# Kernel tuning notes

Hardware: AMD Instinct MI355X
Metric: run time of the kernel (lower is better)

## Reference

```python
import jax, jax.numpy as jnp
import numpy as np

N_NODES = 50000
N_EDGES = 800000
D_IN = 128
D_HID = 256
N_CLASSES = 2
N_GRAPHS = 256


def _graph_conv(x, src, dst, W_root, W_rel, b, num_nodes):
    # PyG GraphConv: out_i = W_root @ x_i + W_rel @ sum_{j->i} x_j + b
    agg = jax.ops.segment_sum(x[src], dst, num_segments=num_nodes)  # [N, d_in]
    return x @ W_root.T + agg @ W_rel.T + b


def setup_inputs() -> dict:
    key = jax.random.key(0)
    ks = jax.random.split(key, 12)
    x = jax.random.normal(ks[0], (N_NODES, D_IN), dtype=jnp.float32)
    edge_index = jax.random.randint(ks[1], (2, N_EDGES), 0, N_NODES, dtype=jnp.int64)
    batch = jnp.sort(jax.random.randint(ks[2], (N_NODES,), 0, N_GRAPHS, dtype=jnp.int64))
    s1 = 1.0 / np.sqrt(D_IN)
    s2 = 1.0 / np.sqrt(D_HID)
    W1_root = jax.random.uniform(ks[3], (D_HID, D_IN), minval=-s1, maxval=s1, dtype=jnp.float32)
    W1_rel = jax.random.uniform(ks[4], (D_HID, D_IN), minval=-s1, maxval=s1, dtype=jnp.float32)
    b1 = jax.random.uniform(ks[5], (D_HID,), minval=-s1, maxval=s1, dtype=jnp.float32)
    W2_root = jax.random.uniform(ks[6], (D_HID, D_HID), minval=-s2, maxval=s2, dtype=jnp.float32)
    W2_rel = jax.random.uniform(ks[7], (D_HID, D_HID), minval=-s2, maxval=s2, dtype=jnp.float32)
    b2 = jax.random.uniform(ks[8], (D_HID,), minval=-s2, maxval=s2, dtype=jnp.float32)
    Wfc = jax.random.uniform(ks[9], (N_CLASSES, D_HID), minval=-s2, maxval=s2, dtype=jnp.float32)
    bfc = jax.random.uniform(ks[10], (N_CLASSES,), minval=-s2, maxval=s2, dtype=jnp.float32)
    return {"x": x, "edge_index": edge_index, "batch": batch, "num_graphs": N_GRAPHS,
            "W1_root": W1_root, "W1_rel": W1_rel, "b1": b1,
            "W2_root": W2_root, "W2_rel": W2_rel, "b2": b2,
            "Wfc": Wfc, "bfc": bfc}


def reference(x, edge_index, batch, num_graphs, W1_root, W1_rel, b1, W2_root, W2_rel, b2, Wfc, bfc):
    src, dst = edge_index[0], edge_index[1]
    n = x.shape[0]
    h = jax.nn.relu(_graph_conv(x, src, dst, W1_root, W1_rel, b1, n))
    h = jax.nn.relu(_graph_conv(h, src, dst, W2_root, W2_rel, b2, n))
    # global mean pool over graph segments
    sums = jax.ops.segment_sum(h, batch, num_segments=num_graphs)        # [G, d]
    counts = jax.ops.segment_sum(jnp.ones((n,), h.dtype), batch, num_segments=num_graphs)
    pooled = sums / jnp.maximum(counts, 1.0)[:, None]
    logits = pooled @ Wfc.T + bfc
    return jax.nn.sigmoid(logits)
```

## Files before the change

### kernel.cpp

```cpp
#include <hip/hip_runtime.h>
#include <math.h>

#define D_IN 128
#define D_HID 256
#define N_CLASSES 2
#define N_GRAPHS 256
#define BUCKET 64

#define PSZ  256
#define NP   196
#define CAP  4608
#define LCAP 64
#define EPB  4096

typedef __attribute__((ext_vector_type(8))) short short8;
typedef __attribute__((ext_vector_type(4))) float float4v;

__device__ __forceinline__ unsigned short f2bf(float f) {
    union { float f; unsigned int u; } v; v.f = f;
    unsigned int r = v.u + 0x7FFFu + ((v.u >> 16) & 1u);
    return (unsigned short)(r >> 16);
}
__device__ __forceinline__ float bf2f(unsigned short h) {
    union { unsigned int u; float f; } v; v.u = ((unsigned int)h) << 16;
    return v.f;
}

#define GLD_LDS16(gp, lp) __builtin_amdgcn_global_load_lds( \
    (const __attribute__((address_space(1))) void*)(gp),    \
    (__attribute__((address_space(3))) void*)(lp), 16, 0, 0)

__global__ void prep_kernel(const int* __restrict__ src, const int* __restrict__ dst,
                            int E, int nba,
                            int* __restrict__ pcnt, unsigned int* __restrict__ part,
                            const float* __restrict__ x,
                            const float* __restrict__ w1r, const float* __restrict__ w1a,
                            const float* __restrict__ w2r, const float* __restrict__ w2a,
                            unsigned short* __restrict__ xb,
                            unsigned short* __restrict__ o1r, unsigned short* __restrict__ o1a,
                            unsigned short* __restrict__ o2r, unsigned short* __restrict__ o2a,
                            int n4x) {
    __shared__ int lcnt[NP];
    __shared__ int lbase[NP];
    __shared__ unsigned int stage[NP][LCAP];

    const int tid = threadIdx.x;

    if (blockIdx.x >= nba) {
        int i = (blockIdx.x - nba) * 256 + tid;
        const float* in; unsigned short* out; int off;
        if (i < n4x)                 { in = x;   out = xb;  off = i; }
        else {
            int j = i - n4x;
            if (j < 8192)            { in = w1r; out = o1r; off = j; }
            else if (j < 16384)      { in = w1a; out = o1a; off = j - 8192; }
            else if (j < 32768)      { in = w2r; out = o2r; off = j - 16384; }
            else if (j < 49152)      { in = w2a; out = o2a; off = j - 32768; }
            else return;
        }
        float4 v = ((const float4*)in)[off];
        ushort4 o;
        o.x = f2bf(v.x); o.y = f2bf(v.y); o.z = f2bf(v.z); o.w = f2bf(v.w);
        ((ushort4*)out)[off] = o;
        return;
    }

    for (int p = tid; p < NP; p += 256) lcnt[p] = 0;
    __syncthreads();

    const int e0 = blockIdx.x * EPB;
    const int e1 = min(E, e0 + EPB);
    for (int e = e0 + tid; e < e1; e += 256) {
        int s = src[e];
        int d = dst[e];
        int p = d >> 8;
        unsigned int v = ((unsigned int)(d & (PSZ - 1)) << 16) | (unsigned int)s;
        int pos = atomicAdd(&lcnt[p], 1);
        if (pos < LCAP) stage[p][pos] = v;
        else {
            int g = atomicAdd(&pcnt[p], 1);
            if (g < CAP) part[(size_t)p * CAP + g] = v;
        }
    }
    __syncthreads();

    for (int p = tid; p < NP; p += 256) {
        int nn = min(lcnt[p], LCAP);
        lbase[p] = atomicAdd(&pcnt[p], nn);
    }
    __syncthreads();

    const int wv = tid >> 6, lane = tid & 63;
    for (int p = wv; p < NP; p += 4) {
        const int nn = min(lcnt[p], LCAP);
        const int b = lbase[p];
        for (int i = lane; i < nn; i += 64) {
            int g = b + i;
            if (g < CAP) part[(size_t)p * CAP + g] = stage[p][i];
        }
    }
}

__global__ void bucket_kernel(const unsigned int* __restrict__ part,
                              const int* __restrict__ pcnt,
                              int* __restrict__ cursor,
                              unsigned short* __restrict__ srcs, int N) {
    __shared__ int lcur[PSZ];
    __shared__ __align__(16) unsigned short lsrc[PSZ][BUCKET];

    const int p = blockIdx.x;
    const int tid = threadIdx.x;

    lcur[tid] = 0;
    __syncthreads();

    const int n = min(pcnt[p], CAP);
    const unsigned int* pp = part + (size_t)p * CAP;
    for (int i = tid; i < n; i += 256) {
        unsigned int v = pp[i];
        int dl = v >> 16;
        int pos = atomicAdd(&lcur[dl], 1);
        if (pos < BUCKET) lsrc[dl][pos] = (unsigned short)(v & 0xFFFFu);
    }
    __syncthreads();

    const int nodeBase = p * PSZ;
    if (nodeBase + tid < N) cursor[nodeBase + tid] = lcur[tid];

    const uint4* ls = (const uint4*)&lsrc[0][0];
    uint4* gs = (uint4*)(srcs + (size_t)nodeBase * BUCKET);
#pragma unroll
    for (int i = tid; i < PSZ * BUCKET / 8; i += 256) {
        if (nodeBase + (i >> 3) < N) gs[i] = ls[i];
    }
}

template <int D>
__global__ void gather_bucket_bf16(const unsigned short* __restrict__ feat,
                                   const unsigned short* __restrict__ srcs,
                                   const int* __restrict__ cnt,
                                   unsigned short* __restrict__ agg, int N) {
    const int wave = (blockIdx.x * blockDim.x + threadIdx.x) >> 6;
    const int lane = threadIdx.x & 63;
    if (wave >= N) return;
    const unsigned short* bucket = srcs + (size_t)wave * BUCKET;
    int my = bucket[lane];
    const int c = min(cnt[wave], BUCKET);

    if (D == 256) {
        float a0 = 0.f, a1 = 0.f, a2 = 0.f, a3 = 0.f;
        float b0 = 0.f, b1 = 0.f, b2 = 0.f, b3 = 0.f;
        const unsigned short* base = feat + lane * 4;
        int i = 0;
        for (; i + 4 <= c; i += 4) {
            int s0 = __shfl(my, i + 0);
            int s1 = __shfl(my, i + 1);
            int s2 = __shfl(my, i + 2);
            int s3 = __shfl(my, i + 3);
            uint2 w0 = *(const uint2*)(base + (size_t)s0 * 256);
            uint2 w1 = *(const uint2*)(base + (size_t)s1 * 256);
            uint2 w2 = *(const uint2*)(base + (size_t)s2 * 256);
            uint2 w3 = *(const uint2*)(base + (size_t)s3 * 256);
            a0 += bf2f((unsigned short)(w0.x & 0xFFFF)); a1 += bf2f((unsigned short)(w0.x >> 16));
            a2 += bf2f((unsigned short)(w0.y & 0xFFFF)); a3 += bf2f((unsigned short)(w0.y >> 16));
            b0 += bf2f((unsigned short)(w1.x & 0xFFFF)); b1 += bf2f((unsigned short)(w1.x >> 16));
            b2 += bf2f((unsigned short)(w1.y & 0xFFFF)); b3 += bf2f((unsigned short)(w1.y >> 16));
            a0 += bf2f((unsigned short)(w2.x & 0xFFFF)); a1 += bf2f((unsigned short)(w2.x >> 16));
            a2 += bf2f((unsigned short)(w2.y & 0xFFFF)); a3 += bf2f((unsigned short)(w2.y >> 16));
            b0 += bf2f((unsigned short)(w3.x & 0xFFFF)); b1 += bf2f((unsigned short)(w3.x >> 16));
            b2 += bf2f((unsigned short)(w3.y & 0xFFFF)); b3 += bf2f((unsigned short)(w3.y >> 16));
        }
        for (; i < c; i++) {
            int s = __shfl(my, i);
            uint2 w = *(const uint2*)(base + (size_t)s * 256);
            a0 += bf2f((unsigned short)(w.x & 0xFFFF)); a1 += bf2f((unsigned short)(w.x >> 16));
            a2 += bf2f((unsigned short)(w.y & 0xFFFF)); a3 += bf2f((unsigned short)(w.y >> 16));
        }
        a0 += b0; a1 += b1; a2 += b2; a3 += b3;
        uint2 o;
        o.x = (unsigned int)f2bf(a0) | ((unsigned int)f2bf(a1) << 16);
        o.y = (unsigned int)f2bf(a2) | ((unsigned int)f2bf(a3) << 16);
        *(uint2*)(agg + (size_t)wave * 256 + lane * 4) = o;
    } else {
        const int half = lane >> 5;
        const int hl = lane & 31;
        float a0 = 0.f, a1 = 0.f, a2 = 0.f, a3 = 0.f;
        float b0 = 0.f, b1 = 0.f, b2 = 0.f, b3 = 0.f;
        const unsigned short* base = feat + hl * 4;
        int i = 0;
        for (; i + 4 <= c; i += 4) {
            int sA = __shfl(my, i + half);
            int sB = __shfl(my, i + 2 + half);
            uint2 wA = *(const uint2*)(base + (size_t)sA * 128);
            uint2 wB = *(const uint2*)(base + (size_t)sB * 128);
            a0 += bf2f((unsigned short)(wA.x & 0xFFFF)); a1 += bf2f((unsigned short)(wA.x >> 16));
            a2 += bf2f((unsigned short)(wA.y & 0xFFFF)); a3 += bf2f((unsigned short)(wA.y >> 16));
            b0 += bf2f((unsigned short)(wB.x & 0xFFFF)); b1 += bf2f((unsigned short)(wB.x >> 16));
            b2 += bf2f((unsigned short)(wB.y & 0xFFFF)); b3 += bf2f((unsigned short)(wB.y >> 16));
        }
        for (; i < c; i += 2) {
            if (i + half < c) {
                int s = __shfl(my, i + half);
                uint2 w = *(const uint2*)(base + (size_t)s * 128);
                a0 += bf2f((unsigned short)(w.x & 0xFFFF)); a1 += bf2f((unsigned short)(w.x >> 16));
                a2 += bf2f((unsigned short)(w.y & 0xFFFF)); a3 += bf2f((unsigned short)(w.y >> 16));
            }
        }
        a0 += b0; a1 += b1; a2 += b2; a3 += b3;
        a0 += __shfl_xor(a0, 32);
        a1 += __shfl_xor(a1, 32);
        a2 += __shfl_xor(a2, 32);
        a3 += __shfl_xor(a3, 32);
        if (half == 0) {
            uint2 o;
            o.x = (unsigned int)f2bf(a0) | ((unsigned int)f2bf(a1) << 16);
            o.y = (unsigned int)f2bf(a2) | ((unsigned int)f2bf(a3) << 16);
            *(uint2*)(agg + (size_t)wave * 128 + hl * 4) = o;
        }
    }
}

template <int K1>
__global__ void gemm_mfma_dual(const unsigned short* __restrict__ X,
                               const unsigned short* __restrict__ Ag,
                               const unsigned short* __restrict__ Wr,
                               const unsigned short* __restrict__ Wa,
                               const float* __restrict__ bias,
                               unsigned short* __restrict__ out,
                               int Nrows) {
    __shared__ __align__(16) unsigned short As[128][32];
    __shared__ __align__(16) unsigned short Bs[256][32];

    const int tid = threadIdx.x;
    const int w = tid >> 6;
    const int lane = tid & 63;
    const int quad = lane >> 4;
    const int r16 = lane & 15;
    const int srow = lane >> 2;
    const int scol = (lane & 3) * 8;
    const int i0 = blockIdx.x * 128;
    const int m0 = (w >> 2) * 64;
    const int n0 = (w & 3) * 64;

    float4v acc[4][4];
#pragma unroll
    for (int mt = 0; mt < 4; mt++)
#pragma unroll
        for (int nt = 0; nt < 4; nt++) {
            float4v z = {0.f, 0.f, 0.f, 0.f};
            acc[mt][nt] = z;
        }

    for (int k0 = 0; k0 < 2 * K1; k0 += 32) {
        const bool first = (k0 < K1);
        const int kb = first ? k0 : (k0 - K1);
        const unsigned short* PA = first ? X : Ag;
        const unsigned short* PB = first ? Wr : Wa;

        {
            const int rr = w * 16;
            GLD_LDS16(PA + (size_t)(i0 + rr + srow) * K1 + kb + scol, &As[rr][0]);
        }
#pragma unroll
        for (int t = 0; t < 2; t++) {
            const int rr = w * 32 + t * 16;
            GLD_LDS16(PB + (size_t)(rr + srow) * K1 + kb + scol, &Bs[rr][0]);
        }
        __syncthreads();

        short8 af[4], bfr[4];
#pragma unroll
        for (int mt = 0; mt < 4; mt++)
            af[mt] = *(const short8*)&As[m0 + mt * 16 + r16][quad * 8];
#pragma unroll
        for (int nt = 0; nt < 4; nt++)
            bfr[nt] = *(const short8*)&Bs[n0 + nt * 16 + r16][quad * 8];
#pragma unroll
        for (int mt = 0; mt < 4; mt++)
#pragma unroll
            for (int nt = 0; nt < 4; nt++)
                acc[mt][nt] = __builtin_amdgcn_mfma_f32_16x16x32_bf16(
                    af[mt], bfr[nt], acc[mt][nt], 0, 0, 0);
        __syncthreads();
    }

#pragma unroll
    for (int mt = 0; mt < 4; mt++) {
#pragma unroll
        for (int e = 0; e < 4; e++) {
            const int m = i0 + m0 + mt * 16 + quad * 4 + e;
            if (m >= Nrows) continue;
#pragma unroll
            for (int nt = 0; nt < 4; nt++) {
                const int n = n0 + nt * 16 + r16;
                float v = acc[mt][nt][e] + bias[n];
                out[(size_t)m * 256 + n] = f2bf(fmaxf(v, 0.f));
            }
        }
    }
}

__global__ void pool_fc_kernel(const unsigned short* __restrict__ h,
                               const int* __restrict__ batch,
                               const float* __restrict__ Wfc,
                               const float* __restrict__ bfc,
                               float* __restrict__ out,
                               int N) {
    const int g = blockIdx.x;
    const int tid = threadIdx.x;
    const int wv = tid >> 6;
    const int lane = tid & 63;

    int lo = 0, hi = N;
    while (lo < hi) { int mid = (lo + hi) >> 1; if (batch[mid] < g) lo = mid + 1; else hi = mid; }
    const int start = lo;
    hi = N;
    while (lo < hi) { int mid = (lo + hi) >> 1; if (batch[mid] < g + 1) lo = mid + 1; else hi = mid; }
    const int end = lo;

    float a0 = 0.f, a1 = 0.f, a2 = 0.f, a3 = 0.f;
    float b0 = 0.f, b1 = 0.f, b2 = 0.f, b3 = 0.f;
    const unsigned short* base = h + lane * 4;
    int r = start + wv;
    for (; r + 16 < end; r += 32) {
        uint2 wA = *(const uint2*)(base + (size_t)r * 256);
        uint2 wB = *(const uint2*)(base + (size_t)(r + 16) * 256);
        a0 += bf2f((unsigned short)(wA.x & 0xFFFF)); a1 += bf2f((unsigned short)(wA.x >> 16));
        a2 += bf2f((unsigned short)(wA.y & 0xFFFF)); a3 += bf2f((unsigned short)(wA.y >> 16));
        b0 += bf2f((unsigned short)(wB.x & 0xFFFF)); b1 += bf2f((unsigned short)(wB.x >> 16));
        b2 += bf2f((unsigned short)(wB.y & 0xFFFF)); b3 += bf2f((unsigned short)(wB.y >> 16));
    }
    if (r < end) {
        uint2 wA = *(const uint2*)(base + (size_t)r * 256);
        a0 += bf2f((unsigned short)(wA.x & 0xFFFF)); a1 += bf2f((unsigned short)(wA.x >> 16));
        a2 += bf2f((unsigned short)(wA.y & 0xFFFF)); a3 += bf2f((unsigned short)(wA.y >> 16));
    }
    a0 += b0; a1 += b1; a2 += b2; a3 += b3;

    __shared__ float part[16][D_HID];
    part[wv][lane * 4 + 0] = a0;
    part[wv][lane * 4 + 1] = a1;
    part[wv][lane * 4 + 2] = a2;
    part[wv][lane * 4 + 3] = a3;
    __syncthreads();

    __shared__ float pooled[D_HID];
    __shared__ float red[2 * D_HID];
    if (tid < D_HID) {
        float s = 0.f;
#pragma unroll
        for (int w2 = 0; w2 < 16; w2++) s += part[w2][tid];
        const float cnt = fmaxf((float)(end - start), 1.0f);
        pooled[tid] = s / cnt;
    }
    __syncthreads();

    if (tid < 2 * D_HID) {
        const int c = tid >> 8;
        const int col = tid & 255;
        red[tid] = pooled[col] * Wfc[c * D_HID + col];
    }
    __syncthreads();
    for (int off = D_HID / 2; off > 0; off >>= 1) {
        if (tid < 2 * D_HID && (tid & 255) < off) red[tid] += red[tid + off];
        __syncthreads();
    }
    if (tid < N_CLASSES) {
        float logit = red[tid << 8] + bfc[tid];
        out[g * N_CLASSES + tid] = 1.0f / (1.0f + expf(-logit));
    }
}

extern "C" void kernel_launch(void* const* d_in, const int* in_sizes, int n_in,
                              void* d_out, int out_size, void* d_ws, size_t ws_size,
                              hipStream_t stream) {
    const float* x     = (const float*)d_in[0];
    const int*   edge  = (const int*)d_in[1];
    const int*   batch = (const int*)d_in[2];
    const float* W1r = (const float*)d_in[4];
    const float* W1a = (const float*)d_in[5];
    const float* b1  = (const float*)d_in[6];
    const float* W2r = (const float*)d_in[7];
    const float* W2a = (const float*)d_in[8];
    const float* b2  = (const float*)d_in[9];
    const float* Wfc = (const float*)d_in[10];
    const float* bfc = (const float*)d_in[11];

    const int N = in_sizes[0] / D_IN;
    const int E = in_sizes[1] / 2;
    const int* src = edge;
    const int* dst = edge + E;

    unsigned short* xb    = (unsigned short*)d_ws;
    unsigned short* agg1b = xb    + (size_t)N * 128;
    unsigned short* h1b   = agg1b + (size_t)N * 128;
    unsigned short* agg2b = h1b   + (size_t)N * 256;
    unsigned short* h2b   = agg2b + (size_t)N * 256;
    unsigned short* w1r_b = h2b   + (size_t)N * 256;
    unsigned short* w1a_b = w1r_b + 256 * 128;
    unsigned short* w2r_b = w1a_b + 256 * 128;
    unsigned short* w2a_b = w2r_b + 256 * 256;
    int* cursor = (int*)(w2a_b + 256 * 256);
    unsigned short* srcs = (unsigned short*)(cursor + N);
    int* pcnt = (int*)(srcs + (size_t)N * BUCKET);

    unsigned int* part = (unsigned int*)h2b;

    hipMemsetAsync(pcnt, 0, NP * sizeof(int), stream);

    const int nba = (E + EPB - 1) / EPB;
    const int n4x = N * D_IN / 4;
    const int cvtBlocks = (n4x + 49152 + 255) / 256;
    prep_kernel<<<nba + cvtBlocks, 256, 0, stream>>>(
        src, dst, E, nba, pcnt, part,
        x, W1r, W1a, W2r, W2a, xb, w1r_b, w1a_b, w2r_b, w2a_b, n4x);

    bucket_kernel<<<NP, 256, 0, stream>>>(part, pcnt, cursor, srcs, N);

    gather_bucket_bf16<D_IN><<<(N + 3) / 4, 256, 0, stream>>>(xb, srcs, cursor, agg1b, N);
    gemm_mfma_dual<D_IN><<<(N + 127) / 128, 512, 0, stream>>>(
        xb, agg1b, w1r_b, w1a_b, b1, h1b, N);

    gather_bucket_bf16<D_HID><<<(N + 3) / 4, 256, 0, stream>>>(h1b, srcs, cursor, agg2b, N);
    gemm_mfma_dual<D_HID><<<(N + 127) / 128, 512, 0, stream>>>(
        h1b, agg2b, w2r_b, w2a_b, b2, h2b, N);

    pool_fc_kernel<<<N_GRAPHS, 1024, 0, stream>>>(h2b, batch, Wfc, bfc, (float*)d_out, N);
}
```

Before: 252.2 us.

## Fuse neighbor gather into dual GEMM, keeping aggregates in shared memory

After: 273.0 us. 8.2% more time.

```diff
diff --git a/kernel.cpp b/kernel.cpp
--- a/kernel.cpp
+++ b/kernel.cpp
@@ -135,116 +135,123 @@
     }
 }
 
-template <int D>
-__global__ void gather_bucket_bf16(const unsigned short* __restrict__ feat,
-                                   const unsigned short* __restrict__ srcs,
-                                   const int* __restrict__ cnt,
-                                   unsigned short* __restrict__ agg, int N) {
-    const int wave = (blockIdx.x * blockDim.x + threadIdx.x) >> 6;
-    const int lane = threadIdx.x & 63;
-    if (wave >= N) return;
-    const unsigned short* bucket = srcs + (size_t)wave * BUCKET;
-    int my = bucket[lane];
-    const int c = min(cnt[wave], BUCKET);
-
-    if (D == 256) {
-        float a0 = 0.f, a1 = 0.f, a2 = 0.f, a3 = 0.f;
-        float b0 = 0.f, b1 = 0.f, b2 = 0.f, b3 = 0.f;
-        const unsigned short* base = feat + lane * 4;
-        int i = 0;
-        for (; i + 4 <= c; i += 4) {
-            int s0 = __shfl(my, i + 0);
-            int s1 = __shfl(my, i + 1);
-            int s2 = __shfl(my, i + 2);
-            int s3 = __shfl(my, i + 3);
-            uint2 w0 = *(const uint2*)(base + (size_t)s0 * 256);
-            uint2 w1 = *(const uint2*)(base + (size_t)s1 * 256);
-            uint2 w2 = *(const uint2*)(base + (size_t)s2 * 256);
-            uint2 w3 = *(const uint2*)(base + (size_t)s3 * 256);
-            a0 += bf2f((unsigned short)(w0.x & 0xFFFF)); a1 += bf2f((unsigned short)(w0.x >> 16));
-            a2 += bf2f((unsigned short)(w0.y & 0xFFFF)); a3 += bf2f((unsigned short)(w0.y >> 16));
-            b0 += bf2f((unsigned short)(w1.x & 0xFFFF)); b1 += bf2f((unsigned short)(w1.x >> 16));
-            b2 += bf2f((unsigned short)(w1.y & 0xFFFF)); b3 += bf2f((unsigned short)(w1.y >> 16));
-            a0 += bf2f((unsigned short)(w2.x & 0xFFFF)); a1 += bf2f((unsigned short)(w2.x >> 16));
-            a2 += bf2f((unsigned short)(w2.y & 0xFFFF)); a3 += bf2f((unsigned short)(w2.y >> 16));
-            b0 += bf2f((unsigned short)(w3.x & 0xFFFF)); b1 += bf2f((unsigned short)(w3.x >> 16));
-            b2 += bf2f((unsigned short)(w3.y & 0xFFFF)); b3 += bf2f((unsigned short)(w3.y >> 16));
-        }
-        for (; i < c; i++) {
-            int s = __shfl(my, i);
-            uint2 w = *(const uint2*)(base + (size_t)s * 256);
-            a0 += bf2f((unsigned short)(w.x & 0xFFFF)); a1 += bf2f((unsigned short)(w.x >> 16));
-            a2 += bf2f((unsigned short)(w.y & 0xFFFF)); a3 += bf2f((unsigned short)(w.y >> 16));
-        }
-        a0 += b0; a1 += b1; a2 += b2; a3 += b3;
-        uint2 o;
-        o.x = (unsigned int)f2bf(a0) | ((unsigned int)f2bf(a1) << 16);
-        o.y = (unsigned int)f2bf(a2) | ((unsigned int)f2bf(a3) << 16);
-        *(uint2*)(agg + (size_t)wave * 256 + lane * 4) = o;
-    } else {
-        const int half = lane >> 5;
-        const int hl = lane & 31;
-        float a0 = 0.f, a1 = 0.f, a2 = 0.f, a3 = 0.f;
-        float b0 = 0.f, b1 = 0.f, b2 = 0.f, b3 = 0.f;
-        const unsigned short* base = feat + hl * 4;
-        int i = 0;
-        for (; i + 4 <= c; i += 4) {
-            int sA = __shfl(my, i + half);
-            int sB = __shfl(my, i + 2 + half);
-            uint2 wA = *(const uint2*)(base + (size_t)sA * 128);
-            uint2 wB = *(const uint2*)(base + (size_t)sB * 128);
-            a0 += bf2f((unsigned short)(wA.x & 0xFFFF)); a1 += bf2f((unsigned short)(wA.x >> 16));
-            a2 += bf2f((unsigned short)(wA.y & 0xFFFF)); a3 += bf2f((unsigned short)(wA.y >> 16));
-            b0 += bf2f((unsigned short)(wB.x & 0xFFFF)); b1 += bf2f((unsigned short)(wB.x >> 16));
-            b2 += bf2f((unsigned short)(wB.y & 0xFFFF)); b3 += bf2f((unsigned short)(wB.y >> 16));
-        }
-        for (; i < c; i += 2) {
-            if (i + half < c) {
-                int s = __shfl(my, i + half);
-                uint2 w = *(const uint2*)(base + (size_t)s * 128);
-                a0 += bf2f((unsigned short)(w.x & 0xFFFF)); a1 += bf2f((unsigned short)(w.x >> 16));
-                a2 += bf2f((unsigned short)(w.y & 0xFFFF)); a3 += bf2f((unsigned short)(w.y >> 16));
+template <int K1>
+__global__ __launch_bounds__(512, 4)
+void fused_gather_gemm(const unsigned short* __restrict__ feat,
+                       const unsigned short* __restrict__ srcs,
+                       const int* __restrict__ cnt,
+                       const unsigned short* __restrict__ Wr,
+                       const unsigned short* __restrict__ Wa,
+                       const float* __restrict__ bias,
+                       unsigned short* __restrict__ out,
+                       int Nrows) {
+    constexpr int NCH = K1 / 32;
+    __shared__ __align__(16) unsigned short aggL[NCH][64][32];
+    __shared__ __align__(16) unsigned short As[64][32];
+    __shared__ __align__(16) unsigned short Bs[256][32];
+
+    const int tid = threadIdx.x;
+    const int w = tid >> 6;
+    const int lane = tid & 63;
+    const int i0 = blockIdx.x * 64;
+
+#pragma unroll 1
+    for (int t = 0; t < 8; t++) {
+        const int ml = w * 8 + t;
+        const int m = i0 + ml;
+
+        if (K1 == 256) {
+            float a0 = 0.f, a1 = 0.f, a2 = 0.f, a3 = 0.f;
+            float b0 = 0.f, b1 = 0.f, b2 = 0.f, b3 = 0.f;
+            if (m < Nrows) {
+                int my = srcs[(size_t)m * BUCKET + lane];
+                const int c = min(cnt[m], BUCKET);
+                const unsigned short* base = feat + lane * 4;
+                int i = 0;
+                for (; i + 4 <= c; i += 4) {
+                    int s0 = __shfl(my, i + 0);
+                    int s1 = __shfl(my, i + 1);
+                    int s2 = __shfl(my, i + 2);
+                    int s3 = __shfl(my, i + 3);
+                    uint2 w0 = *(const uint2*)(base + (size_t)s0 * 256);
+                    uint2 w1 = *(const uint2*)(base + (size_t)s1 * 256);
+                    uint2 w2 = *(const uint2*)(base + (size_t)s2 * 256);
+                    uint2 w3 = *(const uint2*)(base + (size_t)s3 * 256);
+                    a0 += bf2f((unsigned short)(w0.x & 0xFFFF)); a1 += bf2f((unsigned short)(w0.x >> 16));
+                    a2 += bf2f((unsigned short)(w0.y & 0xFFFF)); a3 += bf2f((unsigned short)(w0.y >> 16));
+                    b0 += bf2f((unsigned short)(w1.x & 0xFFFF)); b1 += bf2f((unsigned short)(w1.x >> 16));
+                    b2 += bf2f((unsigned short)(w1.y & 0xFFFF)); b3 += bf2f((unsigned short)(w1.y >> 16));
+                    a0 += bf2f((unsigned short)(w2.x & 0xFFFF)); a1 += bf2f((unsigned short)(w2.x >> 16));
+                    a2 += bf2f((unsigned short)(w2.y & 0xFFFF)); a3 += bf2f((unsigned short)(w2.y >> 16));
+                    b0 += bf2f((unsigned short)(w3.x & 0xFFFF)); b1 += bf2f((unsigned short)(w3.x >> 16));
+                    b2 += bf2f((unsigned short)(w3.y & 0xFFFF)); b3 += bf2f((unsigned short)(w3.y >> 16));
+                }
+                for (; i < c; i++) {
+                    int s = __shfl(my, i);
+                    uint2 ww = *(const uint2*)(base + (size_t)s * 256);
+                    a0 += bf2f((unsigned short)(ww.x & 0xFFFF)); a1 += bf2f((unsigned short)(ww.x >> 16));
+                    a2 += bf2f((unsigned short)(ww.y & 0xFFFF)); a3 += bf2f((unsigned short)(ww.y >> 16));
+                }
             }
-        }
-        a0 += b0; a1 += b1; a2 += b2; a3 += b3;
-        a0 += __shfl_xor(a0, 32);
-        a1 += __shfl_xor(a1, 32);
-        a2 += __shfl_xor(a2, 32);
-        a3 += __shfl_xor(a3, 32);
-        if (half == 0) {
+            a0 += b0; a1 += b1; a2 += b2; a3 += b3;
             uint2 o;
             o.x = (unsigned int)f2bf(a0) | ((unsigned int)f2bf(a1) << 16);
             o.y = (unsigned int)f2bf(a2) | ((unsigned int)f2bf(a3) << 16);
-            *(uint2*)(agg + (size_t)wave * 128 + hl * 4) = o;
-        }
-    }
-}
-
-template <int K1>
-__global__ void gemm_mfma_dual(const unsigned short* __restrict__ X,
-                               const unsigned short* __restrict__ Ag,
-                               const unsigned short* __restrict__ Wr,
-                               const unsigned short* __restrict__ Wa,
-                               const float* __restrict__ bias,
-                               unsigned short* __restrict__ out,
-                               int Nrows) {
-    __shared__ __align__(16) unsigned short As[128][32];
-    __shared__ __align__(16) unsigned short Bs[256][32];
-
-    const int tid = threadIdx.x;
-    const int w = tid >> 6;
-    const int lane = tid & 63;
+            *(uint2*)&aggL[lane >> 3][ml][(lane & 7) * 4] = o;
+        } else {
+            const int half = lane >> 5;
+            const int hl = lane & 31;
+            float a0 = 0.f, a1 = 0.f, a2 = 0.f, a3 = 0.f;
+            float b0 = 0.f, b1 = 0.f, b2 = 0.f, b3 = 0.f;
+            if (m < Nrows) {
+                int my = srcs[(size_t)m * BUCKET + lane];
+                const int c = min(cnt[m], BUCKET);
+                const unsigned short* base = feat + hl * 4;
+                int i = 0;
+                for (; i + 4 <= c; i += 4) {
+                    int sA = __shfl(my, i + half);
+                    int sB = __shfl(my, i + 2 + half);
+                    uint2 wA = *(const uint2*)(base + (size_t)sA * 128);
+                    uint2 wB = *(const uint2*)(base + (size_t)sB * 128);
+                    a0 += bf2f((unsigned short)(wA.x & 0xFFFF)); a1 += bf2f((unsigned short)(wA.x >> 16));
+                    a2 += bf2f((unsigned short)(wA.y & 0xFFFF)); a3 += bf2f((unsigned short)(wA.y >> 16));
+                    b0 += bf2f((unsigned short)(wB.x & 0xFFFF)); b1 += bf2f((unsigned short)(wB.x >> 16));
+                    b2 += bf2f((unsigned short)(wB.y & 0xFFFF)); b3 += bf2f((unsigned short)(wB.y >> 16));
+                }
+                for (; i < c; i += 2) {
+                    if (i + half < c) {
+                        int s = __shfl(my, i + half);
+                        uint2 ww = *(const uint2*)(base + (size_t)s * 128);
+                        a0 += bf2f((unsigned short)(ww.x & 0xFFFF)); a1 += bf2f((unsigned short)(ww.x >> 16));
+                        a2 += bf2f((unsigned short)(ww.y & 0xFFFF)); a3 += bf2f((unsigned short)(ww.y >> 16));
+                    }
+                }
+            }
+            a0 += b0; a1 += b1; a2 += b2; a3 += b3;
+            a0 += __shfl_xor(a0, 32);
+            a1 += __shfl_xor(a1, 32);
+            a2 += __shfl_xor(a2, 32);
+            a3 += __shfl_xor(a3, 32);
+            if (half == 0) {
+                uint2 o;
+                o.x = (unsigned int)f2bf(a0) | ((unsigned int)f2bf(a1) << 16);
+                o.y = (unsigned int)f2bf(a2) | ((unsigned int)f2bf(a3) << 16);
+                *(uint2*)&aggL[hl >> 3][ml][(hl & 7) * 4] = o;
+            }
+        }
+    }
+    __syncthreads();
+
     const int quad = lane >> 4;
     const int r16 = lane & 15;
     const int srow = lane >> 2;
     const int scol = (lane & 3) * 8;
-    const int i0 = blockIdx.x * 128;
-    const int m0 = (w >> 2) * 64;
+    const int m0 = (w >> 2) * 32;
     const int n0 = (w & 3) * 64;
 
-    float4v acc[4][4];
-#pragma unroll
-    for (int mt = 0; mt < 4; mt++)
+    float4v acc[2][4];
+#pragma unroll
+    for (int mt = 0; mt < 2; mt++)
 #pragma unroll
         for (int nt = 0; nt < 4; nt++) {
             float4v z = {0.f, 0.f, 0.f, 0.f};
@@ -254,12 +261,11 @@
     for (int k0 = 0; k0 < 2 * K1; k0 += 32) {
         const bool first = (k0 < K1);
         const int kb = first ? k0 : (k0 - K1);
-        const unsigned short* PA = first ? X : Ag;
         const unsigned short* PB = first ? Wr : Wa;
 
-        {
+        if (first && w < 4) {
             const int rr = w * 16;
-            GLD_LDS16(PA + (size_t)(i0 + rr + srow) * K1 + kb + scol, &As[rr][0]);
+            GLD_LDS16(feat + (size_t)(i0 + rr + srow) * K1 + kb + scol, &As[rr][0]);
         }
 #pragma unroll
         for (int t = 0; t < 2; t++) {
@@ -268,15 +274,16 @@
         }
         __syncthreads();
 
-        short8 af[4], bfr[4];
-#pragma unroll
-        for (int mt = 0; mt < 4; mt++)
-            af[mt] = *(const short8*)&As[m0 + mt * 16 + r16][quad * 8];
+        short8 af[2], bfr[4];
+#pragma unroll
+        for (int mt = 0; mt < 2; mt++)
+            af[mt] = first ? *(const short8*)&As[m0 + mt * 16 + r16][quad * 8]
+                           : *(const short8*)&aggL[kb >> 5][m0 + mt * 16 + r16][quad * 8];
 #pragma unroll
         for (int nt = 0; nt < 4; nt++)
             bfr[nt] = *(const short8*)&Bs[n0 + nt * 16 + r16][quad * 8];
 #pragma unroll
-        for (int mt = 0; mt < 4; mt++)
+        for (int mt = 0; mt < 2; mt++)
 #pragma unroll
             for (int nt = 0; nt < 4; nt++)
                 acc[mt][nt] = __builtin_amdgcn_mfma_f32_16x16x32_bf16(
@@ -285,7 +292,7 @@
     }
 
 #pragma unroll
-    for (int mt = 0; mt < 4; mt++) {
+    for (int mt = 0; mt < 2; mt++) {
 #pragma unroll
         for (int e = 0; e < 4; e++) {
             const int m = i0 + m0 + mt * 16 + quad * 4 + e;
@@ -417,13 +424,12 @@
 
     bucket_kernel<<<NP, 256, 0, stream>>>(part, pcnt, cursor, srcs, N);
 
-    gather_bucket_bf16<D_IN><<<(N + 3) / 4, 256, 0, stream>>>(xb, srcs, cursor, agg1b, N);
-    gemm_mfma_dual<D_IN><<<(N + 127) / 128, 512, 0, stream>>>(
-        xb, agg1b, w1r_b, w1a_b, b1, h1b, N);
-
-    gather_bucket_bf16<D_HID><<<(N + 3) / 4, 256, 0, stream>>>(h1b, srcs, cursor, agg2b, N);
-    gemm_mfma_dual<D_HID><<<(N + 127) / 128, 512, 0, stream>>>(
-        h1b, agg2b, w2r_b, w2a_b, b2, h2b, N);
+    const int nblk = (N + 63) / 64;
+    fused_gather_gemm<D_IN><<<nblk, 512, 0, stream>>>(
+        xb, srcs, cursor, w1r_b, w1a_b, b1, h1b, N);
+
+    fused_gather_gemm<D_HID><<<nblk, 512, 0, stream>>>(
+        h1b, srcs, cursor, w2r_b, w2a_b, b2, h2b, N);
 
     pool_fc_kernel<<<N_GRAPHS, 1024, 0, stream>>>(h2b, batch, Wfc, bfc, (float*)d_out, N);
 }
```

## Fuse mean-pool accumulation into second GraphConv GEMM epilogue

Applied to the files above, without the earlier changes.

After: 322.1 us. 1.28x slower.

```diff
diff --git a/kernel.cpp b/kernel.cpp
--- a/kernel.cpp
+++ b/kernel.cpp
@@ -12,6 +12,7 @@
 #define CAP  4608
 #define LCAP 64
 #define EPB  4096
+#define GSPAN 8
 
 typedef __attribute__((ext_vector_type(8))) short short8;
 typedef __attribute__((ext_vector_type(4))) float float4v;
@@ -300,73 +301,129 @@
     }
 }
 
-__global__ void pool_fc_kernel(const unsigned short* __restrict__ h,
+__global__ void gemm_pool_mfma(const unsigned short* __restrict__ X,
+                               const unsigned short* __restrict__ Ag,
+                               const unsigned short* __restrict__ Wr,
+                               const unsigned short* __restrict__ Wa,
+                               const float* __restrict__ bias,
                                const int* __restrict__ batch,
-                               const float* __restrict__ Wfc,
-                               const float* __restrict__ bfc,
-                               float* __restrict__ out,
-                               int N) {
+                               float* __restrict__ pooledG,
+                               int Nrows) {
+    constexpr int K1 = D_HID;
+    __shared__ __align__(16) unsigned short As[128][32];
+    __shared__ __align__(16) unsigned short Bs[256][32];
+    __shared__ float pp[GSPAN][256];
+
+    const int tid = threadIdx.x;
+    const int w = tid >> 6;
+    const int lane = tid & 63;
+    const int quad = lane >> 4;
+    const int r16 = lane & 15;
+    const int srow = lane >> 2;
+    const int scol = (lane & 3) * 8;
+    const int i0 = blockIdx.x * 128;
+    const int m0 = (w >> 2) * 64;
+    const int n0 = (w & 3) * 64;
+
+    for (int i = tid; i < GSPAN * 256; i += 512) ((float*)pp)[i] = 0.f;
+
+    float4v acc[4][4];
+#pragma unroll
+    for (int mt = 0; mt < 4; mt++)
+#pragma unroll
+        for (int nt = 0; nt < 4; nt++) {
+            float4v z = {0.f, 0.f, 0.f, 0.f};
+            acc[mt][nt] = z;
+        }
+
+    for (int k0 = 0; k0 < 2 * K1; k0 += 32) {
+        const bool first = (k0 < K1);
+        const int kb = first ? k0 : (k0 - K1);
+        const unsigned short* PA = first ? X : Ag;
+        const unsigned short* PB = first ? Wr : Wa;
+
+        {
+            const int rr = w * 16;
+            GLD_LDS16(PA + (size_t)(i0 + rr + srow) * K1 + kb + scol, &As[rr][0]);
+        }
+#pragma unroll
+        for (int t = 0; t < 2; t++) {
+            const int rr = w * 32 + t * 16;
+            GLD_LDS16(PB + (size_t)(rr + srow) * K1 + kb + scol, &Bs[rr][0]);
+        }
+        __syncthreads();
+
+        short8 af[4], bfr[4];
+#pragma unroll
+        for (int mt = 0; mt < 4; mt++)
+            af[mt] = *(const short8*)&As[m0 + mt * 16 + r16][quad * 8];
+#pragma unroll
+        for (int nt = 0; nt < 4; nt++)
+            bfr[nt] = *(const short8*)&Bs[n0 + nt * 16 + r16][quad * 8];
+#pragma unroll
+        for (int mt = 0; mt < 4; mt++)
+#pragma unroll
+            for (int nt = 0; nt < 4; nt++)
+                acc[mt][nt] = __builtin_amdgcn_mfma_f32_16x16x32_bf16(
+                    af[mt], bfr[nt], acc[mt][nt], 0, 0, 0);
+        __syncthreads();
+    }
+
+    const int g0 = batch[i0];
+#pragma unroll
+    for (int mt = 0; mt < 4; mt++) {
+#pragma unroll
+        for (int e = 0; e < 4; e++) {
+            const int m = i0 + m0 + mt * 16 + quad * 4 + e;
+            if (m >= Nrows) continue;
+            const int gl = batch[m] - g0;
+#pragma unroll
+            for (int nt = 0; nt < 4; nt++) {
+                const int n = n0 + nt * 16 + r16;
+                float v = fmaxf(acc[mt][nt][e] + bias[n], 0.f);
+                if (gl < GSPAN) atomicAdd(&pp[gl][n], v);
+                else            atomicAdd(&pooledG[(size_t)(g0 + gl) * 256 + n], v);
+            }
+        }
+    }
+    __syncthreads();
+
+    const int col = tid & 255;
+    const int gh = tid >> 8;
+#pragma unroll
+    for (int t = 0; t < GSPAN / 2; t++) {
+        const int gl = gh * (GSPAN / 2) + t;
+        float v = pp[gl][col];
+        if (v != 0.f) atomicAdd(&pooledG[(size_t)(g0 + gl) * 256 + col], v);
+    }
+}
+
+__global__ void finalize_fc(const float* __restrict__ pooledG,
+                            const int* __restrict__ batch,
+                            const float* __restrict__ Wfc,
+                            const float* __restrict__ bfc,
+                            float* __restrict__ out, int N) {
     const int g = blockIdx.x;
     const int tid = threadIdx.x;
-    const int wv = tid >> 6;
-    const int lane = tid & 63;
 
     int lo = 0, hi = N;
     while (lo < hi) { int mid = (lo + hi) >> 1; if (batch[mid] < g) lo = mid + 1; else hi = mid; }
     const int start = lo;
     hi = N;
     while (lo < hi) { int mid = (lo + hi) >> 1; if (batch[mid] < g + 1) lo = mid + 1; else hi = mid; }
-    const int end = lo;
-
-    float a0 = 0.f, a1 = 0.f, a2 = 0.f, a3 = 0.f;
-    float b0 = 0.f, b1 = 0.f, b2 = 0.f, b3 = 0.f;
-    const unsigned short* base = h + lane * 4;
-    int r = start + wv;
-    for (; r + 16 < end; r += 32) {
-        uint2 wA = *(const uint2*)(base + (size_t)r * 256);
-        uint2 wB = *(const uint2*)(base + (size_t)(r + 16) * 256);
-        a0 += bf2f((unsigned short)(wA.x & 0xFFFF)); a1 += bf2f((unsigned short)(wA.x >> 16));
-        a2 += bf2f((unsigned short)(wA.y & 0xFFFF)); a3 += bf2f((unsigned short)(wA.y >> 16));
-        b0 += bf2f((unsigned short)(wB.x & 0xFFFF)); b1 += bf2f((unsigned short)(wB.x >> 16));
-        b2 += bf2f((unsigned short)(wB.y & 0xFFFF)); b3 += bf2f((unsigned short)(wB.y >> 16));
-    }
-    if (r < end) {
-        uint2 wA = *(const uint2*)(base + (size_t)r * 256);
-        a0 += bf2f((unsigned short)(wA.x & 0xFFFF)); a1 += bf2f((unsigned short)(wA.x >> 16));
-        a2 += bf2f((unsigned short)(wA.y & 0xFFFF)); a3 += bf2f((unsigned short)(wA.y >> 16));
-    }
-    a0 += b0; a1 += b1; a2 += b2; a3 += b3;
-
-    __shared__ float part[16][D_HID];
-    part[wv][lane * 4 + 0] = a0;
-    part[wv][lane * 4 + 1] = a1;
-    part[wv][lane * 4 + 2] = a2;
-    part[wv][lane * 4 + 3] = a3;
-    __syncthreads();
-
-    __shared__ float pooled[D_HID];
-    __shared__ float red[2 * D_HID];
-    if (tid < D_HID) {
-        float s = 0.f;
-#pragma unroll
-        for (int w2 = 0; w2 < 16; w2++) s += part[w2][tid];
-        const float cnt = fmaxf((float)(end - start), 1.0f);
-        pooled[tid] = s / cnt;
-    }
-    __syncthreads();
-
-    if (tid < 2 * D_HID) {
-        const int c = tid >> 8;
-        const int col = tid & 255;
-        red[tid] = pooled[col] * Wfc[c * D_HID + col];
-    }
-    __syncthreads();
-    for (int off = D_HID / 2; off > 0; off >>= 1) {
-        if (tid < 2 * D_HID && (tid & 255) < off) red[tid] += red[tid + off];
+    const float cnt = fmaxf((float)(lo - start), 1.0f);
+
+    __shared__ float red0[256], red1[256];
+    const float pm = pooledG[(size_t)g * 256 + tid] / cnt;
+    red0[tid] = pm * Wfc[tid];
+    red1[tid] = pm * Wfc[256 + tid];
+    __syncthreads();
+    for (int off = 128; off > 0; off >>= 1) {
+        if (tid < off) { red0[tid] += red0[tid + off]; red1[tid] += red1[tid + off]; }
         __syncthreads();
     }
     if (tid < N_CLASSES) {
-        float logit = red[tid << 8] + bfc[tid];
+        float logit = (tid == 0 ? red0[0] : red1[0]) + bfc[tid];
         out[g * N_CLASSES + tid] = 1.0f / (1.0f + expf(-logit));
     }
 }
@@ -403,10 +460,12 @@
     int* cursor = (int*)(w2a_b + 256 * 256);
     unsigned short* srcs = (unsigned short*)(cursor + N);
     int* pcnt = (int*)(srcs + (size_t)N * BUCKET);
+    float* pooledG = (float*)(pcnt + NP);
 
     unsigned int* part = (unsigned int*)h2b;
 
     hipMemsetAsync(pcnt, 0, NP * sizeof(int), stream);
+    hipMemsetAsync(pooledG, 0, (size_t)N_GRAPHS * 256 * sizeof(float), stream);
 
     const int nba = (E + EPB - 1) / EPB;
     const int n4x = N * D_IN / 4;
@@ -422,8 +481,8 @@
         xb, agg1b, w1r_b, w1a_b, b1, h1b, N);
 
     gather_bucket_bf16<D_HID><<<(N + 3) / 4, 256, 0, stream>>>(h1b, srcs, cursor, agg2b, N);
-    gemm_mfma_dual<D_HID><<<(N + 127) / 128, 512, 0, stream>>>(
-        h1b, agg2b, w2r_b, w2a_b, b2, h2b, N);
-
-    pool_fc_kernel<<<N_GRAPHS, 1024, 0, stream>>>(h2b, batch, Wfc, bfc, (float*)d_out, N);
-}
+    gemm_pool_mfma<<<(N + 127) / 128, 512, 0, stream>>>(
+        h1b, agg2b, w2r_b, w2a_b, b2, batch, pooledG, N);
+
+    finalize_fc<<<N_GRAPHS, 256, 0, stream>>>(pooledG, batch, Wfc, bfc, (float*)d_out, N);
+}
```
